# Kernel tuning notes

Measured on AMD Instinct MI355X. Metric: run time of the kernel, lower is better.

Reference implementation:

```python
import jax, jax.numpy as jnp
import numpy as np

N = 65536  # number of points
# (out_ch, in_ch) for the 8 shared-MLP (1x1-conv) blocks
_DIMS = [(64, 3), (64, 64), (128, 64), (1024, 128), (512, 1088), (256, 512), (128, 256), (1, 128)]


def setup_inputs() -> dict:
    key = jax.random.key(0)
    ks = jax.random.split(key, 1 + 2 * len(_DIMS))
    inp = {"x": jax.random.normal(ks[0], (1, 1, N, 3), jnp.float32)}
    for i, (o, c) in enumerate(_DIMS):
        scale = 1.0 / np.sqrt(c)
        inp[f"W{i+1}"] = jax.random.normal(ks[1 + 2 * i], (o, c), jnp.float32) * scale
        inp[f"b{i+1}"] = jax.random.uniform(ks[2 + 2 * i], (o,), jnp.float32, -scale, scale)
    return inp


def reference(x, W1, b1, W2, b2, W3, b3, W4, b4, W5, b5, W6, b6, W7, b7, W8, b8):
    # x: [1,1,n,3]. Conv2d with kernel [1,3] over the width-3 axis == per-point linear on xyz.
    pts = x[0, 0]                                   # [n,3]
    n = pts.shape[0]
    h = jax.nn.relu(pts @ W1.T + b1)                # [n,64]   block1
    h = jax.nn.relu(h @ W2.T + b2)                  # [n,64]   block2 (kept for skip-concat)
    y = jax.nn.relu(h @ W3.T + b3)                  # [n,128]  block3
    y = jax.nn.relu(y @ W4.T + b4)                  # [n,1024] block4
    g = jnp.max(y, axis=0)                          # [1024]   global max-pool over points
    # broadcast global feature to every point and concat with per-point features -> [n,1088]
    feat = jnp.concatenate([h, jnp.broadcast_to(g, (n, g.shape[0]))], axis=1)
    z = jax.nn.relu(feat @ W5.T + b5)               # [n,512]
    z = jax.nn.relu(z @ W6.T + b6)                  # [n,256]
    z = jax.nn.relu(z @ W7.T + b7)                  # [n,128]
    z = z @ W8.T + b8                               # [n,1]    block8 (no relu)
    return z.reshape(1, 1, n, 1)
```

## Files before the change

### kernel.cpp

```cpp
#include <hip/hip_runtime.h>

#define NPTS 65536

typedef __bf16 bf16_t;
typedef __bf16 bf16x8 __attribute__((ext_vector_type(8)));
typedef float f32x16 __attribute__((ext_vector_type(16)));

#define MFMA32(A, B, C) __builtin_amdgcn_mfma_f32_32x32x16_bf16(A, B, C, 0, 0, 0)

__device__ __forceinline__ float relu(float v) { return v > 0.f ? v : 0.f; }


struct PrepSeg { const float* src; bf16_t* h; bf16_t* l; int SW; int K; int nblk; };
struct PrepAll { PrepSeg seg[6]; };

__global__ __launch_bounds__(256) void kprep(PrepAll pa) {
  int blk = blockIdx.x, i = 0;
  while (blk >= pa.seg[i].nblk) { blk -= pa.seg[i].nblk; ++i; }
  const PrepSeg sg = pa.seg[i];
  int t8 = blk * 256 + threadIdx.x;
  int l = t8 & 63;
  int rest = t8 >> 6;
  int NKC = sg.K >> 4;
  int kc = rest % NKC, st = rest / NKC;
  int n = st * 32 + (l & 31);
  int k0 = kc * 16 + (l >> 5) * 8;
  const float* src = sg.src + (size_t)n * sg.SW + k0;
  bf16x8 hv, lv;
#pragma unroll
  for (int j = 0; j < 8; ++j) {
    float v = src[j];
    bf16_t h = (bf16_t)v;
    hv[j] = h; lv[j] = (bf16_t)(v - (float)h);
  }
  *(bf16x8*)(sg.h + (size_t)t8 * 8) = hv;
  *(bf16x8*)(sg.l + (size_t)t8 * 8) = lv;
}

__global__ __launch_bounds__(256, 2) void k1a(
    const float* __restrict__ x, const float* __restrict__ W1, const float* __restrict__ b1,
    bf16_t* __restrict__ h1h, bf16_t* __restrict__ h1l) {
  int p = blockIdx.x * 256 + threadIdx.x;
  float x0 = x[p * 3 + 0], x1 = x[p * 3 + 1], x2 = x[p * 3 + 2];
  int b = p >> 7, mi = (p >> 5) & 3, p31 = p & 31;
#pragma unroll
  for (int kc = 0; kc < 4; ++kc)
#pragma unroll
    for (int hbw = 0; hbw < 2; ++hbw) {
      bf16x8 hv, lv;
#pragma unroll
      for (int j = 0; j < 8; ++j) {
        int c = kc * 16 + hbw * 8 + j;
        float v = relu(fmaf(W1[c * 3], x0, fmaf(W1[c * 3 + 1], x1, fmaf(W1[c * 3 + 2], x2, b1[c]))));
        bf16_t h = (bf16_t)v;
        hv[j] = h; lv[j] = (bf16_t)(v - (float)h);
      }
      size_t off = (((size_t)(b * 4 + kc) * 4 + mi) * 64 + hbw * 32 + p31) * 8;
      *(bf16x8*)(h1h + off) = hv;
      *(bf16x8*)(h1l + off) = lv;
    }
}

template <int PB, int K, int MODE>
__global__ __launch_bounds__(256, 3) void gemmS(
    const bf16_t* __restrict__ Ah, const bf16_t* __restrict__ Al,
    const bf16_t* __restrict__ Wh, const bf16_t* __restrict__ Wl,
    const float* __restrict__ bias, int nko,
    bf16_t* __restrict__ Oh, bf16_t* __restrict__ Ol,
    float* __restrict__ aux, const float* __restrict__ w8, const float* __restrict__ b8) {
  constexpr int WC = 4 / PB;
  constexpr int NKC = K / 16;
  constexpr int KG = 2;
  constexpr int NG = NKC / KG;
  __shared__ bf16_t smem[2][PB][2][KG * 2048];

  int tid = threadIdx.x;
  int lane = tid & 63;
  int w = __builtin_amdgcn_readfirstlane(tid >> 6);
  int rg = w / WC, cw = w % WC;
  int hb = lane >> 5, p31 = lane & 31;
  int bx = blockIdx.x;
  int st0 = blockIdx.y * WC + cw;
  int bblk = bx * PB + rg;

  f32x16 acc[4];
#pragma unroll
  for (int r = 0; r < 16; ++r) {
    float bv = bias[st0 * 32 + 8 * (r >> 2) + 4 * hb + (r & 3)];
#pragma unroll
    for (int mi = 0; mi < 4; ++mi) acc[mi][r] = bv;
  }

  auto stage = [&](int buf, int g) {
#pragma unroll
    for (int i = 0; i < PB * 4; ++i) {
      int u = i * 256 + tid;
      int rgs = u >> 10, rem = u & 1023;
      int t = rem >> 9, inner = rem & 511;
      const bf16_t* src = (t ? Al : Ah) +
          ((size_t)(bx * PB + rgs) * NKC + g * KG) * 2048 + inner * 8;
      *(bf16x8*)&smem[buf][rgs][t][inner * 8] = *(const bf16x8*)src;
    }
  };

  bf16x8 wch[KG], wcl[KG], wnh[KG], wnl[KG];
  auto wload = [&](int g, bf16x8* h, bf16x8* l) {
#pragma unroll
    for (int kcl = 0; kcl < KG; ++kcl) {
      size_t wo = (((size_t)st0 * NKC + g * KG + kcl) * 64 + lane) * 8;
      h[kcl] = *(const bf16x8*)(Wh + wo);
      l[kcl] = *(const bf16x8*)(Wl + wo);
    }
  };

  auto compute = [&](int buf, bf16x8* h, bf16x8* l) {
#pragma unroll
    for (int kcl = 0; kcl < KG; ++kcl)
#pragma unroll
      for (int mi = 0; mi < 4; ++mi) {
        const bf16_t* xp = &smem[buf][rg][0][((kcl * 4 + mi) * 64 + lane) * 8];
        bf16x8 xh = *(const bf16x8*)xp;
        bf16x8 xl = *(const bf16x8*)(xp + KG * 2048);
        acc[mi] = MFMA32(h[kcl], xh, acc[mi]);
        acc[mi] = MFMA32(l[kcl], xh, acc[mi]);
        acc[mi] = MFMA32(h[kcl], xl, acc[mi]);
      }
  };

  stage(0, 0);
  wload(0, wch, wcl);
  for (int g = 0; g < NG; ++g) {
    __syncthreads();
    if (g + 1 < NG) {
      stage((g + 1) & 1, g + 1);
      wload(g + 1, wnh, wnl);
    }
    compute(g & 1, wch, wcl);
#pragma unroll
    for (int kcl = 0; kcl < KG; ++kcl) { wch[kcl] = wnh[kcl]; wcl[kcl] = wnl[kcl]; }
  }

  if constexpr (MODE == 0) {
#pragma unroll
    for (int mi = 0; mi < 4; ++mi) {
      float a[16], rcv[8];
#pragma unroll
      for (int r = 0; r < 16; ++r) a[r] = relu(acc[mi][r]);
#pragma unroll
      for (int j = 0; j < 8; ++j) rcv[j] = __shfl_xor(hb ? a[j] : a[8 + j], 32);
      float o0[8], o1[8];
#pragma unroll
      for (int j = 0; j < 4; ++j) {
        o0[j]     = hb ? rcv[j]     : a[j];
        o0[4 + j] = hb ? a[8 + j]   : rcv[j];
        o1[j]     = hb ? rcv[4 + j] : a[4 + j];
        o1[4 + j] = hb ? a[12 + j]  : rcv[4 + j];
      }
      bf16x8 h0, l0, h1, l1;
#pragma unroll
      for (int j = 0; j < 8; ++j) {
        bf16_t x0 = (bf16_t)o0[j]; h0[j] = x0; l0[j] = (bf16_t)(o0[j] - (float)x0);
        bf16_t x1 = (bf16_t)o1[j]; h1[j] = x1; l1[j] = (bf16_t)(o1[j] - (float)x1);
      }
      int kco = st0 * 2 + hb;
      size_t ob = ((size_t)(bblk * nko + kco) * 4 + mi) * 64;
      *(bf16x8*)(Oh + (ob + p31) * 8)      = h0;
      *(bf16x8*)(Ol + (ob + p31) * 8)      = l0;
      *(bf16x8*)(Oh + (ob + 32 + p31) * 8) = h1;
      *(bf16x8*)(Ol + (ob + 32 + p31) * 8) = l1;
    }
  } else if constexpr (MODE == 1) {
#pragma unroll
    for (int r = 0; r < 16; ++r) {
      float m = relu(acc[0][r]);
#pragma unroll
      for (int mi = 1; mi < 4; ++mi) m = fmaxf(m, relu(acc[mi][r]));
#pragma unroll
      for (int off = 1; off < 32; off <<= 1) m = fmaxf(m, __shfl_xor(m, off));
      if (p31 == 0)
        aux[(size_t)bx * 1024 + st0 * 32 + 8 * (r >> 2) + 4 * hb + (r & 3)] = m;
    }
  } else {
    __shared__ float sp[4][128];
    float w8v[16];
#pragma unroll
    for (int r = 0; r < 16; ++r) w8v[r] = w8[st0 * 32 + 8 * (r >> 2) + 4 * hb + (r & 3)];
#pragma unroll
    for (int mi = 0; mi < 4; ++mi) {
      float s = 0.f;
#pragma unroll
      for (int r = 0; r < 16; ++r) s = fmaf(relu(acc[mi][r]), w8v[r], s);
      s += __shfl_xor(s, 32);
      if (hb == 0) sp[w][mi * 32 + p31] = s;
    }
    __syncthreads();
    if (tid < 128)
      aux[(size_t)bx * 128 + tid] = sp[0][tid] + sp[1][tid] + sp[2][tid] + sp[3][tid] + b8[0];
  }
}

__global__ __launch_bounds__(256) void kgmax(const float* __restrict__ gpart, float* __restrict__ g) {
  int t = blockIdx.x * 256 + threadIdx.x;
  int c = t & 1023, rg = t >> 10;
  const float* gp = gpart + (size_t)rg * 64 * 1024 + c;
  float m = 0.f;
#pragma unroll 8
  for (int r = 0; r < 64; ++r) m = fmaxf(m, gp[(size_t)r * 1024]);
  atomicMax((unsigned int*)(g + c), __float_as_uint(m));
}

__global__ __launch_bounds__(256) void kc5(
    const float* __restrict__ W5, const float* __restrict__ b5,
    const float* __restrict__ g, float* __restrict__ c5) {
  int tid = threadIdx.x;
  int ci = tid >> 3, kg = tid & 7;
  int c = blockIdx.x * 32 + ci;
  const float* wrow = W5 + (size_t)c * 1088 + 64 + kg * 128;
  const float* gp = g + kg * 128;
  float acc = 0.f;
#pragma unroll 8
  for (int k = 0; k < 128; ++k) acc += wrow[k] * gp[k];
#pragma unroll
  for (int off = 1; off <= 4; off <<= 1) acc += __shfl_xor(acc, off);
  if (kg == 0) c5[c] = acc + b5[c];
}


struct Oct { bf16x8 h0, l0, h1, l1; };
__device__ __forceinline__ Oct epi_pack(const f32x16& accv, int hb) {
  float a[16], rcv[8];
#pragma unroll
  for (int r = 0; r < 16; ++r) a[r] = relu(accv[r]);
#pragma unroll
  for (int j = 0; j < 8; ++j) rcv[j] = __shfl_xor(hb ? a[j] : a[8 + j], 32);
  float o0[8], o1[8];
#pragma unroll
  for (int j = 0; j < 4; ++j) {
    o0[j]     = hb ? rcv[j]     : a[j];
    o0[4 + j] = hb ? a[8 + j]   : rcv[j];
    o1[j]     = hb ? rcv[4 + j] : a[4 + j];
    o1[4 + j] = hb ? a[12 + j]  : rcv[4 + j];
  }
  Oct o;
#pragma unroll
  for (int j = 0; j < 8; ++j) {
    bf16_t x0 = (bf16_t)o0[j]; o.h0[j] = x0; o.l0[j] = (bf16_t)(o0[j] - (float)x0);
    bf16_t x1 = (bf16_t)o1[j]; o.h1[j] = x1; o.l1[j] = (bf16_t)(o1[j] - (float)x1);
  }
  return o;
}

__device__ __forceinline__ void epi_store_lds(const Oct& o, bf16_t* H, bf16_t* L, int ob, int p31) {
  *(bf16x8*)(H + (ob + p31) * 8)      = o.h0;
  *(bf16x8*)(H + (ob + 32 + p31) * 8) = o.h1;
  *(bf16x8*)(L + (ob + p31) * 8)      = o.l0;
  *(bf16x8*)(L + (ob + 32 + p31) * 8) = o.l1;
}

__device__ __forceinline__ void binit2(f32x16 acc[2], const float* bias, int base, int hb) {
#pragma unroll
  for (int r = 0; r < 16; ++r) {
    float bv = bias[base + 8 * (r >> 2) + 4 * hb + (r & 3)];
    acc[0][r] = bv; acc[1][r] = bv;
  }
}

template <int NKC>
__device__ __forceinline__ void wgemm(const bf16_t* __restrict__ Wh, const bf16_t* __restrict__ Wl,
                                      int st, const bf16_t* act, int loOff, int lane,
                                      f32x16 acc[2]) {
#pragma unroll
  for (int kc = 0; kc < NKC; ++kc) {
    size_t wo = ((size_t)(st * NKC + kc) * 64 + lane) * 8;
    bf16x8 awh = *(const bf16x8*)(Wh + wo), awl = *(const bf16x8*)(Wl + wo);
    bf16x8 xh[2], xl[2];
#pragma unroll
    for (int mi = 0; mi < 2; ++mi) {
      const bf16_t* xp = act + ((kc * 2 + mi) * 64 + lane) * 8;
      xh[mi] = *(const bf16x8*)xp; xl[mi] = *(const bf16x8*)(xp + loOff);
    }
#pragma unroll
    for (int mi = 0; mi < 2; ++mi) acc[mi] = MFMA32(awh, xh[mi], acc[mi]);
#pragma unroll
    for (int mi = 0; mi < 2; ++mi) acc[mi] = MFMA32(awl, xh[mi], acc[mi]);
#pragma unroll
    for (int mi = 0; mi < 2; ++mi) acc[mi] = MFMA32(awh, xl[mi], acc[mi]);
  }
}

__global__ __launch_bounds__(256, 2) void mega2(
    const bf16_t* __restrict__ h2gh, const bf16_t* __restrict__ h2gl,
    const bf16_t* __restrict__ W5h, const bf16_t* __restrict__ W5l, const float* __restrict__ c5,
    const bf16_t* __restrict__ W6h, const bf16_t* __restrict__ W6l, const float* __restrict__ b6,
    const bf16_t* __restrict__ W7h, const bf16_t* __restrict__ W7l, const float* __restrict__ b7,
    const float* __restrict__ w8, const float* __restrict__ b8v, float* __restrict__ out) {
  __shared__ __align__(16) bf16_t smem[32768];
  __shared__ float sp[4][64];
  int tid = threadIdx.x, lane = tid & 63;
  int w = __builtin_amdgcn_readfirstlane(tid >> 6);
  int hb = lane >> 5, p31 = lane & 31;
  int b = blockIdx.x;
  int B = b >> 1, half = b & 1;
  bf16_t* z5buf = smem + 8192;

#pragma unroll
  for (int i = 0; i < 4; ++i) {
    int u = i * 256 + tid;
    int t = u >> 9, rem = u & 511;
    int kcmi = rem >> 6, l = rem & 63;
    int kc = kcmi >> 1, mi2 = kcmi & 1;
    size_t so = ((size_t)((B * 4 + kc) * 4 + half * 2 + mi2) * 64 + l) * 8;
    const bf16_t* src = (t ? h2gl : h2gh) + so;
    *(bf16x8*)(smem + t * 4096 + rem * 8) = *(const bf16x8*)src;
  }
  __syncthreads();

  f32x16 z6a[2][2];
#pragma unroll
  for (int s = 0; s < 2; ++s)
#pragma unroll
    for (int r = 0; r < 16; ++r) {
      float bv = b6[(w * 2 + s) * 32 + 8 * (r >> 2) + 4 * hb + (r & 3)];
      z6a[s][0][r] = bv; z6a[s][1][r] = bv;
    }

  for (int g5 = 0; g5 < 4; ++g5) {
    int st5 = g5 * 4 + w;
    f32x16 a5[2];
    binit2(a5, c5, st5 * 32, hb);
    wgemm<4>(W5h, W5l, st5, smem, 4096, lane, a5);
    __syncthreads();
#pragma unroll
    for (int mi = 0; mi < 2; ++mi) {
      Oct o = epi_pack(a5[mi], hb);
      epi_store_lds(o, z5buf, z5buf + 8192, ((w * 2 + hb) * 2 + mi) * 64, p31);
    }
    __syncthreads();
#pragma unroll
    for (int kc = 0; kc < 8; ++kc) {
      bf16x8 awh[2], awl[2], xh[2], xl[2];
#pragma unroll
      for (int s = 0; s < 2; ++s) {
        size_t wo = ((size_t)((w * 2 + s) * 32 + g5 * 8 + kc) * 64 + lane) * 8;
        awh[s] = *(const bf16x8*)(W6h + wo);
        awl[s] = *(const bf16x8*)(W6l + wo);
      }
#pragma unroll
      for (int mi = 0; mi < 2; ++mi) {
        const bf16_t* xp = z5buf + ((kc * 2 + mi) * 64 + lane) * 8;
        xh[mi] = *(const bf16x8*)xp; xl[mi] = *(const bf16x8*)(xp + 8192);
      }
#pragma unroll
      for (int s = 0; s < 2; ++s)
#pragma unroll
        for (int mi = 0; mi < 2; ++mi) z6a[s][mi] = MFMA32(awh[s], xh[mi], z6a[s][mi]);
#pragma unroll
      for (int s = 0; s < 2; ++s)
#pragma unroll
        for (int mi = 0; mi < 2; ++mi) z6a[s][mi] = MFMA32(awl[s], xh[mi], z6a[s][mi]);
#pragma unroll
      for (int s = 0; s < 2; ++s)
#pragma unroll
        for (int mi = 0; mi < 2; ++mi) z6a[s][mi] = MFMA32(awh[s], xl[mi], z6a[s][mi]);
    }
  }
  __syncthreads();
#pragma unroll
  for (int s = 0; s < 2; ++s) {
    int kcb = (w * 2 + s) * 2 + hb;
#pragma unroll
    for (int mi = 0; mi < 2; ++mi) {
      Oct o = epi_pack(z6a[s][mi], hb);
      epi_store_lds(o, smem, smem + 16384, (kcb * 2 + mi) * 64, p31);
    }
  }
  __syncthreads();
  f32x16 a7[2];
  binit2(a7, b7, w * 32, hb);
  wgemm<16>(W7h, W7l, w, smem, 16384, lane, a7);
  float w8v[16];
#pragma unroll
  for (int r = 0; r < 16; ++r) w8v[r] = w8[w * 32 + 8 * (r >> 2) + 4 * hb + (r & 3)];
#pragma unroll
  for (int mi = 0; mi < 2; ++mi) {
    float s = 0.f;
#pragma unroll
    for (int r = 0; r < 16; ++r) s = fmaf(relu(a7[mi][r]), w8v[r], s);
    s += __shfl_xor(s, 32);
    if (hb == 0) sp[w][mi * 32 + p31] = s;
  }
  __syncthreads();
  if (tid < 64)
    out[b * 64 + tid] = sp[0][tid] + sp[1][tid] + sp[2][tid] + sp[3][tid] + b8v[0];
}

extern "C" void kernel_launch(void* const* d_in, const int* in_sizes, int n_in,
                              void* d_out, int out_size, void* d_ws, size_t ws_size,
                              hipStream_t stream) {
  const float* x  = (const float*)d_in[0];
  const float* W1 = (const float*)d_in[1];  const float* b1 = (const float*)d_in[2];
  const float* W2 = (const float*)d_in[3];  const float* b2 = (const float*)d_in[4];
  const float* W3 = (const float*)d_in[5];  const float* b3 = (const float*)d_in[6];
  const float* W4 = (const float*)d_in[7];  const float* b4 = (const float*)d_in[8];
  const float* W5 = (const float*)d_in[9];  const float* b5 = (const float*)d_in[10];
  const float* W6 = (const float*)d_in[11]; const float* b6 = (const float*)d_in[12];
  const float* W7 = (const float*)d_in[13]; const float* b7 = (const float*)d_in[14];
  const float* W8 = (const float*)d_in[15]; const float* b8 = (const float*)d_in[16];
  float* out = (float*)d_out;

  const size_t MB = 1ull << 20;
  char* ws = (char*)d_ws;
  bf16_t* h2h = (bf16_t*)(ws + 128 * MB);  bf16_t* h2l = (bf16_t*)(ws + 136 * MB);
  bf16_t* h1h = (bf16_t*)(ws + 144 * MB);  bf16_t* h1l = (bf16_t*)(ws + 152 * MB);
  bf16_t* y3h = (bf16_t*)(ws + 144 * MB);  bf16_t* y3l = (bf16_t*)(ws + 160 * MB);
  float* gpart = (float*)(ws + 208 * MB);
  float* g     = (float*)(ws + 210 * MB);
  float* c5    = (float*)(ws + 210 * MB + 4096);
  char* wb = ws + 210 * MB + 65536;
  bf16_t* W2h = (bf16_t*)(wb);             bf16_t* W2l = (bf16_t*)(wb + 8192);
  bf16_t* W3h = (bf16_t*)(wb + 16384);     bf16_t* W3l = (bf16_t*)(wb + 32768);
  bf16_t* W4h = (bf16_t*)(wb + 49152);     bf16_t* W4l = (bf16_t*)(wb + 311296);
  bf16_t* W5h = (bf16_t*)(wb + 573440);    bf16_t* W5l = (bf16_t*)(wb + 638976);
  bf16_t* W6h = (bf16_t*)(wb + 704512);    bf16_t* W6l = (bf16_t*)(wb + 966656);
  bf16_t* W7h = (bf16_t*)(wb + 1228800);   bf16_t* W7l = (bf16_t*)(wb + 1294336);

  hipMemsetAsync(g, 0, 1024 * sizeof(float), stream);

  PrepAll pa;
  pa.seg[0] = {W2, W2h, W2l, 64, 64, 2};
  pa.seg[1] = {W3, W3h, W3l, 64, 64, 4};
  pa.seg[2] = {W4, W4h, W4l, 128, 128, 64};
  pa.seg[3] = {W5, W5h, W5l, 1088, 64, 16};
  pa.seg[4] = {W6, W6h, W6l, 512, 512, 64};
  pa.seg[5] = {W7, W7h, W7l, 256, 256, 16};
  kprep<<<166, 256, 0, stream>>>(pa);

  k1a<<<256, 256, 0, stream>>>(x, W1, b1, h1h, h1l);
  gemmS<2, 64, 0><<<dim3(256, 1), 256, 0, stream>>>(
      h1h, h1l, W2h, W2l, b2, 4, h2h, h2l, nullptr, nullptr, nullptr);
  gemmS<1, 64, 0><<<dim3(512, 1), 256, 0, stream>>>(
      h2h, h2l, W3h, W3l, b3, 8, y3h, y3l, nullptr, nullptr, nullptr);
  gemmS<1, 128, 1><<<dim3(512, 8), 256, 0, stream>>>(
      y3h, y3l, W4h, W4l, b4, 0, nullptr, nullptr, gpart, nullptr, nullptr);
  kgmax<<<32, 256, 0, stream>>>(gpart, g);
  kc5<<<16, 256, 0, stream>>>(W5, b5, g, c5);
  mega2<<<1024, 256, 0, stream>>>(h2h, h2l, W5h, W5l, c5, W6h, W6l, b6,
                                  W7h, W7l, b7, W8, b8, out);
}
```

Before: 282.5 us.

## Fuse block3 and block4 GEMMs with max-pool into one kernel

Result: slower. 338.7 us (+19.9%).

```diff
diff --git a/kernel.cpp b/kernel.cpp
--- a/kernel.cpp
+++ b/kernel.cpp
@@ -202,10 +202,10 @@
 __global__ __launch_bounds__(256) void kgmax(const float* __restrict__ gpart, float* __restrict__ g) {
   int t = blockIdx.x * 256 + threadIdx.x;
   int c = t & 1023, rg = t >> 10;
-  const float* gp = gpart + (size_t)rg * 64 * 1024 + c;
+  const float* gp = gpart + (size_t)rg * 128 * 1024 + c;
   float m = 0.f;
 #pragma unroll 8
-  for (int r = 0; r < 64; ++r) m = fmaxf(m, gp[(size_t)r * 1024]);
+  for (int r = 0; r < 128; ++r) m = fmaxf(m, gp[(size_t)r * 1024]);
   atomicMax((unsigned int*)(g + c), __float_as_uint(m));
 }
 
@@ -285,6 +285,59 @@
     for (int mi = 0; mi < 2; ++mi) acc[mi] = MFMA32(awl, xh[mi], acc[mi]);
 #pragma unroll
     for (int mi = 0; mi < 2; ++mi) acc[mi] = MFMA32(awh, xl[mi], acc[mi]);
+  }
+}
+
+__global__ __launch_bounds__(256, 3) void m34(
+    const bf16_t* __restrict__ h2gh, const bf16_t* __restrict__ h2gl,
+    const bf16_t* __restrict__ W3h, const bf16_t* __restrict__ W3l, const float* __restrict__ b3,
+    const bf16_t* __restrict__ W4h, const bf16_t* __restrict__ W4l, const float* __restrict__ b4,
+    float* __restrict__ gpart) {
+  __shared__ __align__(16) bf16_t h2s[8192];
+  __shared__ __align__(16) bf16_t y3s[16384];
+  int tid = threadIdx.x, lane = tid & 63;
+  int w = __builtin_amdgcn_readfirstlane(tid >> 6);
+  int hb = lane >> 5, p31 = lane & 31;
+  int b = blockIdx.x;
+  int B = b >> 1, half = b & 1;
+
+#pragma unroll
+  for (int i = 0; i < 4; ++i) {
+    int u = i * 256 + tid;
+    int t = u >> 9, rem = u & 511;
+    int kcmi = rem >> 6, l = rem & 63;
+    int kc = kcmi >> 1, mi2 = kcmi & 1;
+    size_t so = ((size_t)((B * 4 + kc) * 4 + half * 2 + mi2) * 64 + l) * 8;
+    const bf16_t* src = (t ? h2gl : h2gh) + so;
+    *(bf16x8*)(h2s + t * 4096 + rem * 8) = *(const bf16x8*)src;
+  }
+  __syncthreads();
+
+  {
+    f32x16 a3[2];
+    binit2(a3, b3, w * 32, hb);
+    wgemm<4>(W3h, W3l, w, h2s, 4096, lane, a3);
+#pragma unroll
+    for (int mi = 0; mi < 2; ++mi) {
+      Oct o = epi_pack(a3[mi], hb);
+      epi_store_lds(o, y3s, y3s + 8192, ((w * 2 + hb) * 2 + mi) * 64, p31);
+    }
+  }
+  __syncthreads();
+
+  for (int i = 0; i < 8; ++i) {
+    int st4 = i * 4 + w;
+    f32x16 a4[2];
+    binit2(a4, b4, st4 * 32, hb);
+    wgemm<8>(W4h, W4l, st4, y3s, 8192, lane, a4);
+#pragma unroll
+    for (int r = 0; r < 16; ++r) {
+      float m = fmaxf(relu(a4[0][r]), relu(a4[1][r]));
+#pragma unroll
+      for (int off = 1; off < 32; off <<= 1) m = fmaxf(m, __shfl_xor(m, off));
+      if (p31 == 0)
+        gpart[(size_t)b * 1024 + st4 * 32 + 8 * (r >> 2) + 4 * hb + (r & 3)] = m;
+    }
   }
 }
 
@@ -412,8 +465,7 @@
   char* ws = (char*)d_ws;
   bf16_t* h2h = (bf16_t*)(ws + 128 * MB);  bf16_t* h2l = (bf16_t*)(ws + 136 * MB);
   bf16_t* h1h = (bf16_t*)(ws + 144 * MB);  bf16_t* h1l = (bf16_t*)(ws + 152 * MB);
-  bf16_t* y3h = (bf16_t*)(ws + 144 * MB);  bf16_t* y3l = (bf16_t*)(ws + 160 * MB);
-  float* gpart = (float*)(ws + 208 * MB);
+  float* gpart = (float*)(ws + 180 * MB);
   float* g     = (float*)(ws + 210 * MB);
   float* c5    = (float*)(ws + 210 * MB + 4096);
   char* wb = ws + 210 * MB + 65536;
@@ -438,10 +490,7 @@
   k1a<<<256, 256, 0, stream>>>(x, W1, b1, h1h, h1l);
   gemmS<2, 64, 0><<<dim3(256, 1), 256, 0, stream>>>(
       h1h, h1l, W2h, W2l, b2, 4, h2h, h2l, nullptr, nullptr, nullptr);
-  gemmS<1, 64, 0><<<dim3(512, 1), 256, 0, stream>>>(
-      h2h, h2l, W3h, W3l, b3, 8, y3h, y3l, nullptr, nullptr, nullptr);
-  gemmS<1, 128, 1><<<dim3(512, 8), 256, 0, stream>>>(
-      y3h, y3l, W4h, W4l, b4, 0, nullptr, nullptr, gpart, nullptr, nullptr);
+  m34<<<1024, 256, 0, stream>>>(h2h, h2l, W3h, W3l, b3, W4h, W4l, b4, gpart);
   kgmax<<<32, 256, 0, stream>>>(gpart, g);
   kc5<<<16, 256, 0, stream>>>(W5, b5, g, c5);
   mega2<<<1024, 256, 0, stream>>>(h2h, h2l, W5h, W5l, c5, W6h, W6l, b6,
```
